# Kernel tuning notes

Hardware: AMD Instinct MI355X
Metric: run time of the kernel (lower is better)

## Reference

```python
import jax, jax.numpy as jnp
import numpy as np

IN_C, OUT_C, P, K, STRIDE = 256, 256, 4, 3, 1
PAD = (K - 1) // 2

def setup_inputs() -> dict:
    key = jax.random.key(0)
    k1, k2, k3 = jax.random.split(key, 3)
    x = jax.random.normal(k1, (32, IN_C, 64, 64), dtype=jnp.float32)
    # KxK weights for (i,j) pairs where the KxK branch is taken
    Wk = jax.random.normal(k2, (OUT_C, IN_C, K, K), dtype=jnp.float32) * 0.05
    # 1x1 weights (one scalar per (i,j) pair) for the pointwise branch
    W1 = jax.random.normal(k3, (OUT_C, IN_C), dtype=jnp.float32) * 0.05
    return {"x": x, "Wk": Wk, "W1": W1}

def _effective_weight(Wk, W1):
    # Branch selection: j < first_K uses (in_c + j - first_K) % P == 0,
    # else (j - first_K) % P == 0; both equal (j - first_K) mod P == 0
    # with nonnegative modulo, where first_K = i % in_c.
    i = jnp.arange(OUT_C)[:, None]
    j = jnp.arange(IN_C)[None, :]
    first_K = i % IN_C
    kxk_mask = ((j - first_K) % P == 0)  # [out, in] bool
    # 1x1 conv (pad 0, stride s) == center tap of a padded KxK conv (pad (K-1)/2, stride s)
    center = jnp.zeros((K, K), Wk.dtype).at[K // 2, K // 2].set(1.0)
    W_1x1_embedded = W1[:, :, None, None] * center  # [out, in, K, K]
    return jnp.where(kxk_mask[:, :, None, None], Wk, W_1x1_embedded)

def reference(x, Wk, W1):
    W_eff = _effective_weight(Wk, W1)
    out = jax.lax.conv_general_dilated(
        x, W_eff,
        window_strides=(STRIDE, STRIDE),
        padding=[(PAD, PAD), (PAD, PAD)],
        dimension_numbers=("NCHW", "OIHW", "NCHW"),
    )
    return out
```

## Files before the change

kernel.cpp:

```cpp
#include <hip/hip_runtime.h>
#include <hip/hip_bf16.h>


#define IN_C  256
#define OUT_C 256
#define HH    64
#define WW    64

typedef __attribute__((ext_vector_type(8))) short bf16x8;
typedef __attribute__((ext_vector_type(4))) float f32x4;

#define BARC() do {                                              \
        asm volatile("s_waitcnt lgkmcnt(0)" ::: "memory");       \
        __builtin_amdgcn_s_barrier();                            \
        __builtin_amdgcn_sched_barrier(0);                       \
    } while (0)

__device__ __forceinline__ unsigned short f2bf(float f) {
    union { float f; unsigned int u; } v; v.f = f;
    unsigned int r = (v.u + 0x7FFFu + ((v.u >> 16) & 1u)) >> 16;
    return (unsigned short)r;
}

__device__ __forceinline__ unsigned pkbf(float lo, float hi) {
    union { __hip_bfloat162 b; unsigned u; } c;
    c.b = __float22bfloat162_rn(make_float2(lo, hi));
    return c.u;
}

__global__ __launch_bounds__(256)
void hetconv_prep(const float* __restrict__ Wk, const float* __restrict__ W1,
                  unsigned short* __restrict__ ws16) {
    const int TOTAL = 65536 + 131072;
    for (int idx = blockIdx.x * 256 + threadIdx.x; idx < TOTAL; idx += gridDim.x * 256) {
        float f;
        if (idx < 65536) {
            int e = idx & 7, lane = (idx >> 3) & 63, m = (idx >> 9) & 15, ck = idx >> 13;
            int g = ck & 3, h2 = ck >> 2;
            int p = m * 16 + (lane & 15);
            int i = (lane >> 4) * 8 + e;
            int j = g + 4 * (32 * h2 + i);
            int oc = 4 * (p & 63) + (p >> 6);
            f = ((p >> 6) == g) ? Wk[(oc * IN_C + j) * 9 + 4] : W1[oc * IN_C + j];
        } else {
            int k2 = idx - 65536;
            int e = k2 & 7, lane = (k2 >> 3) & 63;
            int mrow = (k2 >> 9) & 1, bi = (k2 >> 10) & 1, tp = (k2 >> 11) & 3;
            int hf = (k2 >> 13) & 1, ck = k2 >> 14;
            int g = ck & 3, h2 = ck >> 2;
            int tf = hf * 4 + tp, tfull = tf < 4 ? tf : tf + 1;
            int lo = bi * 32 + mrow * 16 + (lane & 15);
            int i = (lane >> 4) * 8 + e;
            int oc = 4 * lo + g;
            int j = g + 4 * (32 * h2 + i);
            f = Wk[(oc * IN_C + j) * 9 + tfull];
        }
        ws16[idx] = f2bf(f);
    }
}

__device__ __forceinline__ void stage_x_loads(const float* __restrict__ x, int n, int y0,
                                              int ck, int t, float4 v[4][2]) {
    const int g = ck & 3, h2 = ck >> 2;
    #pragma unroll
    for (int it = 0; it < 4; ++it) {
        int tau = t + it * 256;
        int icp = tau & 15, q = (tau >> 4) & 15, r = tau >> 8;
        int i0 = icp * 2;
        int j0 = g + 4 * (32 * h2 + i0);
        int gy = y0 + r - 1;
        float4 z = {0.f, 0.f, 0.f, 0.f};
        v[it][0] = z; v[it][1] = z;
        if ((unsigned)gy < 64u) {
            const float* p0 = x + (((size_t)n * IN_C + j0) << 12) + (gy << 6) + (q << 2);
            v[it][0] = *(const float4*)p0;
            v[it][1] = *(const float4*)(p0 + 16384);
        }
    }
}

__device__ __forceinline__ void stage_x_writes(int t, float4 v[4][2], unsigned short* __restrict__ xb) {
    #pragma unroll
    for (int it = 0; it < 4; ++it) {
        int tau = t + it * 256;
        int icp = tau & 15, q = (tau >> 4) & 15, r = tau >> 8;
        int i0 = icp * 2;
        unsigned d0 = pkbf(v[it][0].x, v[it][1].x);
        unsigned d1 = pkbf(v[it][0].y, v[it][1].y);
        unsigned d2 = pkbf(v[it][0].z, v[it][1].z);
        unsigned d3 = pkbf(v[it][0].w, v[it][1].w);
        int rb = (r * 66 + q * 4 + 1) * 40 + i0;
        *(unsigned*)&xb[rb]        = d0;
        *(unsigned*)&xb[rb + 40]   = d1;
        *(unsigned*)&xb[rb + 80]   = d2;
        *(unsigned*)&xb[rb + 120]  = d3;
    }
}

__device__ __forceinline__ f32x4 mfma(bf16x8 a, bf16x8 b, f32x4 c) {
    return __builtin_amdgcn_mfma_f32_16x16x32_bf16(a, b, c, 0, 0, 0);
}

__device__ __forceinline__ void partA(const unsigned short* __restrict__ xb,
        const unsigned short* __restrict__ whs, f32x4 acc[8][4],
        int mrow, int ncol, int lrow, int kc, int l) {
    bf16x8 b[4];
    #pragma unroll
    for (int ni = 0; ni < 4; ++ni)
        b[ni] = *(const bf16x8*)&xb[((ncol + 1) * 66 + ni * 16 + lrow + 1) * 40 + kc * 8];
    #pragma unroll
    for (int mi = 0; mi < 8; ++mi) {
        bf16x8 a = *(const bf16x8*)&whs[(mrow + 2 * mi) * 512 + l * 8];
        #pragma unroll
        for (int ni = 0; ni < 4; ++ni)
            acc[mi][ni] = mfma(a, b[ni], acc[mi][ni]);
    }
}

template <int G, int HALF>
__device__ __forceinline__ void taps(const unsigned short* __restrict__ xb,
        const unsigned short* __restrict__ wks, f32x4 acc[8][4],
        int mrow, int ncol, int lrow, int kc, int l) {
    #pragma unroll
    for (int tp = 0; tp < 4; ++tp) {
        const int tfull = HALF ? tp + 5 : tp;
        const int dy = tfull / 3 - 1, dx = tfull % 3 - 1;
        bf16x8 a0 = *(const bf16x8*)&wks[((tp * 2 + 0) * 2 + mrow) * 512 + l * 8];
        bf16x8 a1 = *(const bf16x8*)&wks[((tp * 2 + 1) * 2 + mrow) * 512 + l * 8];
        #pragma unroll
        for (int ni = 0; ni < 4; ++ni) {
            bf16x8 bb = *(const bf16x8*)&xb[((ncol + 1 + dy) * 66 + ni * 16 + lrow + 1 + dx) * 40 + kc * 8];
            acc[2 * G + 0][ni] = mfma(a0, bb, acc[2 * G + 0][ni]);
            acc[2 * G + 1][ni] = mfma(a1, bb, acc[2 * G + 1][ni]);
        }
    }
}

__global__ __launch_bounds__(256, 2)
void hetconv_mfma(const float* __restrict__ x,
                  const unsigned short* __restrict__ wgt,
                  float* __restrict__ out) {
    __shared__ unsigned short xs [4 * 66 * 40];
    __shared__ unsigned short whs[8192];
    __shared__ unsigned short wks[8192];
    const int t    = threadIdx.x;
    const int l    = t & 63;
    const int w    = t >> 6;
    const int mrow = w & 1;
    const int ncol = w >> 1;
    const int lrow = l & 15;
    const int kc   = l >> 4;

    const int bid = blockIdx.x;
    const int n   = (bid & 7) * 4 + (bid >> 8);
    const int y0  = ((bid >> 3) & 31) * 2;

    const unsigned short* WHg = wgt;
    const unsigned short* WKg = wgt + 65536;

    f32x4 acc[8][4];
    #pragma unroll
    for (int mi = 0; mi < 8; ++mi)
        #pragma unroll
        for (int ni = 0; ni < 4; ++ni) acc[mi][ni] = (f32x4){0.f, 0.f, 0.f, 0.f};

    float4 xv[4][2];
    bf16x8 wv[8];

    stage_x_loads(x, n, y0, 0, t, xv);
    #pragma unroll
    for (int it = 0; it < 4; ++it) {
        wv[it]     = *(const bf16x8*)&WHg[(t + it * 256) * 8];
        wv[4 + it] = *(const bf16x8*)&WKg[(t + it * 256) * 8];
    }
    if (t < 128) {
        int r = t >> 5, side = (t >> 4) & 1, u = t & 15;
        *(unsigned*)&xs[(r * 66 + side * 65) * 40 + u * 2] = 0u;
    }
    stage_x_writes(t, xv, xs);
    #pragma unroll
    for (int it = 0; it < 4; ++it) {
        *(bf16x8*)&whs[(t + it * 256) * 8] = wv[it];
        *(bf16x8*)&wks[(t + it * 256) * 8] = wv[4 + it];
    }
    __syncthreads();

#define CHUNK(CK, LAST)                                                          \
    {                                                                            \
        bf16x8 wvb[4];                                                           \
        _Pragma("unroll")                                                        \
        for (int it = 0; it < 4; ++it)     \
            wvb[it] = *(const bf16x8*)&WKg[(CK) * 16384 + 8192 + (t + it * 256) * 8]; \
        partA(xs, whs, acc, mrow, ncol, lrow, kc, l);                            \
        taps<(CK) & 3, 0>(xs, wks, acc, mrow, ncol, lrow, kc, l);                \
        BARC();                                           \
        _Pragma("unroll")                                                        \
        for (int it = 0; it < 4; ++it)                                           \
            *(bf16x8*)&wks[(t + it * 256) * 8] = wvb[it];                        \
        if (!(LAST)) {                               \
            stage_x_loads(x, n, y0, (CK) + 1, t, xv);                            \
            _Pragma("unroll")                                                    \
            for (int it = 0; it < 4; ++it) {                                     \
                wv[it]     = *(const bf16x8*)&WHg[((CK) + 1) * 8192 + (t + it * 256) * 8]; \
                wv[4 + it] = *(const bf16x8*)&WKg[((CK) + 1) * 16384 + (t + it * 256) * 8]; \
            }                                                                    \
        }                                                                        \
        BARC();                                             \
        taps<(CK) & 3, 1>(xs, wks, acc, mrow, ncol, lrow, kc, l);                \
        if (!(LAST)) {                                                           \
            BARC();                                    \
            stage_x_writes(t, xv, xs);                                           \
            _Pragma("unroll")                                                    \
            for (int it = 0; it < 4; ++it) {                                     \
                *(bf16x8*)&whs[(t + it * 256) * 8] = wv[it];                     \
                *(bf16x8*)&wks[(t + it * 256) * 8] = wv[4 + it];                 \
            }                                                                    \
            __syncthreads();                                        \
        }                                                                        \
    }

    CHUNK(0, 0) CHUNK(1, 0) CHUNK(2, 0) CHUNK(3, 0)
    CHUNK(4, 0) CHUNK(5, 0) CHUNK(6, 0) CHUNK(7, 1)
#undef CHUNK

    #pragma unroll
    for (int mi = 0; mi < 8; ++mi) {
        int m = mrow + 2 * mi;
        #pragma unroll
        for (int ni = 0; ni < 4; ++ni) {
            #pragma unroll
            for (int reg = 0; reg < 4; ++reg) {
                int p  = m * 16 + kc * 4 + reg;
                int oc = 4 * (p & 63) + (p >> 6);
                out[(((size_t)n * OUT_C + oc) * HH + (y0 + ncol)) * WW + ni * 16 + lrow] = acc[mi][ni][reg];
            }
        }
    }
}

#define TH 16
#define TW 16
#define ICC 16
__global__ __launch_bounds__(256)
void hetconv_fp32(const float* __restrict__ x,
                  const float* __restrict__ Wk,
                  const float* __restrict__ W1,
                  float* __restrict__ out) {
    const int t    = threadIdx.x;
    const int g    = blockIdx.y;
    const int n    = blockIdx.z;
    const int tile = blockIdx.x;
    const int ty0  = (tile >> 2) * TH;
    const int tx0  = (tile & 3) * TW;
    const int ol = t & 7;
    const int pl = t >> 3;
    const int r  = pl >> 1;
    const int ch = (pl & 1) * 8;
    __shared__ __align__(16) float xsf[ICC * 18 * 20];
    __shared__ __align__(16) float w1s[ICC * 64];
    __shared__ __align__(16) float wksf[4 * 9 * 64];
    float acc[8][8];
    #pragma unroll
    for (int k = 0; k < 8; ++k)
        #pragma unroll
        for (int p = 0; p < 8; ++p) acc[k][p] = 0.f;
    for (int ic0 = 0; ic0 < IN_C; ic0 += ICC) {
        for (int idx = t; idx < ICC * 18 * 18; idx += 256) {
            int ic = idx / 324, rem = idx - ic * 324, rr = rem / 18, cc = rem - rr * 18;
            int gy = ty0 + rr - 1, gx = tx0 + cc - 1;
            float v = 0.f;
            if (gy >= 0 && gy < HH && gx >= 0 && gx < WW)
                v = x[(((size_t)n * IN_C + ic0 + ic) * HH + gy) * WW + gx];
            xsf[ic * 360 + rr * 20 + cc] = v;
        }
        for (int idx = t; idx < ICC * 64; idx += 256) {
            int ic = idx >> 6, o = idx & 63;
            w1s[idx] = W1[(g + 4 * o) * IN_C + ic0 + ic];
        }
        for (int idx = t; idx < 4 * 9 * 64; idx += 256) {
            int a = idx / 576, rem = idx - a * 576, tap = rem >> 6, o = rem & 63;
            wksf[idx] = Wk[((g + 4 * o) * IN_C + ic0 + g + 4 * a) * 9 + tap];
        }
        __syncthreads();
        for (int ic = 0; ic < ICC; ++ic) {
            if ((ic & 3) != g) {
                const float* rowp = &xsf[ic * 360 + (r + 1) * 20 + ch];
                float4 A = *(const float4*)rowp;
                float4 B = *(const float4*)(rowp + 4);
                float  c8 = rowp[8];
                float xv2[8] = {A.y, A.z, A.w, B.x, B.y, B.z, B.w, c8};
                const float* wp = &w1s[ic * 64 + ol * 8];
                float4 wA = *(const float4*)wp;
                float4 wB = *(const float4*)(wp + 4);
                float wv2[8] = {wA.x, wA.y, wA.z, wA.w, wB.x, wB.y, wB.z, wB.w};
                #pragma unroll
                for (int k = 0; k < 8; ++k)
                    #pragma unroll
                    for (int p = 0; p < 8; ++p) acc[k][p] += wv2[k] * xv2[p];
            } else {
                const int a = ic >> 2;
                #pragma unroll
                for (int dy = -1; dy <= 1; ++dy) {
                    const float* rowp = &xsf[ic * 360 + (r + 1 + dy) * 20 + ch];
                    float4 A = *(const float4*)rowp;
                    float4 B = *(const float4*)(rowp + 4);
                    float2 C = *(const float2*)(rowp + 8);
                    float seg[10] = {A.x, A.y, A.z, A.w, B.x, B.y, B.z, B.w, C.x, C.y};
                    #pragma unroll
                    for (int dxi = 0; dxi < 3; ++dxi) {
                        const float* wp = &wksf[(a * 9 + (dy + 1) * 3 + dxi) * 64 + ol * 8];
                        float4 wA = *(const float4*)wp;
                        float4 wB = *(const float4*)(wp + 4);
                        float wv2[8] = {wA.x, wA.y, wA.z, wA.w, wB.x, wB.y, wB.z, wB.w};
                        #pragma unroll
                        for (int k = 0; k < 8; ++k)
                            #pragma unroll
                            for (int p = 0; p < 8; ++p) acc[k][p] += wv2[k] * seg[p + dxi];
                    }
                }
            }
        }
        __syncthreads();
    }
    #pragma unroll
    for (int k = 0; k < 8; ++k) {
        int oc = g + 4 * (ol * 8 + k);
        size_t base = (((size_t)n * OUT_C + oc) * HH + (ty0 + r)) * WW + tx0 + ch;
        float4 v0 = {acc[k][0], acc[k][1], acc[k][2], acc[k][3]};
        float4 v1 = {acc[k][4], acc[k][5], acc[k][6], acc[k][7]};
        *(float4*)(&out[base])     = v0;
        *(float4*)(&out[base + 4]) = v1;
    }
}

extern "C" void kernel_launch(void* const* d_in, const int* in_sizes, int n_in,
                              void* d_out, int out_size, void* d_ws, size_t ws_size,
                              hipStream_t stream) {
    const float* x  = (const float*)d_in[0];
    const float* Wk = (const float*)d_in[1];
    const float* W1 = (const float*)d_in[2];
    float* outp = (float*)d_out;

    if (ws_size >= (size_t)(65536 + 131072) * sizeof(unsigned short)) {
        hetconv_prep<<<256, 256, 0, stream>>>(Wk, W1, (unsigned short*)d_ws);
        hetconv_mfma<<<1024, 256, 0, stream>>>(x, (const unsigned short*)d_ws, outp);
    } else {
        hetconv_fp32<<<dim3(16, 4, 32), 256, 0, stream>>>(x, Wk, W1, outp);
    }
}
```

Before: 118.1 us.

## Shrink LDS x-tile pitch, split B-fragment loads, and restructure chunk staging

```diff
diff --git a/kernel.cpp b/kernel.cpp
--- a/kernel.cpp
+++ b/kernel.cpp
@@ -8,13 +8,8 @@
 #define WW    64
 
 typedef __attribute__((ext_vector_type(8))) short bf16x8;
+typedef __attribute__((ext_vector_type(4))) short bf16x4;
 typedef __attribute__((ext_vector_type(4))) float f32x4;
-
-#define BARC() do {                                              \
-        asm volatile("s_waitcnt lgkmcnt(0)" ::: "memory");       \
-        __builtin_amdgcn_s_barrier();                            \
-        __builtin_amdgcn_sched_barrier(0);                       \
-    } while (0)
 
 __device__ __forceinline__ unsigned short f2bf(float f) {
     union { float f; unsigned int u; } v; v.f = f;
@@ -59,6 +54,9 @@
     }
 }
 
+#define XSPAD 36
+#define XSSZ  (4 * 66 * XSPAD)
+
 __device__ __forceinline__ void stage_x_loads(const float* __restrict__ x, int n, int y0,
                                               int ck, int t, float4 v[4][2]) {
     const int g = ck & 3, h2 = ck >> 2;
@@ -89,12 +87,18 @@
         unsigned d1 = pkbf(v[it][0].y, v[it][1].y);
         unsigned d2 = pkbf(v[it][0].z, v[it][1].z);
         unsigned d3 = pkbf(v[it][0].w, v[it][1].w);
-        int rb = (r * 66 + q * 4 + 1) * 40 + i0;
-        *(unsigned*)&xb[rb]        = d0;
-        *(unsigned*)&xb[rb + 40]   = d1;
-        *(unsigned*)&xb[rb + 80]   = d2;
-        *(unsigned*)&xb[rb + 120]  = d3;
-    }
+        int rb = (r * 66 + q * 4 + 1) * XSPAD + i0;
+        *(unsigned*)&xb[rb]             = d0;
+        *(unsigned*)&xb[rb + XSPAD]     = d1;
+        *(unsigned*)&xb[rb + 2 * XSPAD] = d2;
+        *(unsigned*)&xb[rb + 3 * XSPAD] = d3;
+    }
+}
+
+__device__ __forceinline__ bf16x8 lds_bfrag(const unsigned short* __restrict__ xb, int off) {
+    bf16x4 lo = *(const bf16x4*)&xb[off];
+    bf16x4 hi = *(const bf16x4*)&xb[off + 4];
+    return __builtin_shufflevector(lo, hi, 0, 1, 2, 3, 4, 5, 6, 7);
 }
 
 __device__ __forceinline__ f32x4 mfma(bf16x8 a, bf16x8 b, f32x4 c) {
@@ -107,7 +111,7 @@
     bf16x8 b[4];
     #pragma unroll
     for (int ni = 0; ni < 4; ++ni)
-        b[ni] = *(const bf16x8*)&xb[((ncol + 1) * 66 + ni * 16 + lrow + 1) * 40 + kc * 8];
+        b[ni] = lds_bfrag(xb, ((ncol + 1) * 66 + ni * 16 + lrow + 1) * XSPAD + kc * 8);
     #pragma unroll
     for (int mi = 0; mi < 8; ++mi) {
         bf16x8 a = *(const bf16x8*)&whs[(mrow + 2 * mi) * 512 + l * 8];
@@ -129,7 +133,7 @@
         bf16x8 a1 = *(const bf16x8*)&wks[((tp * 2 + 1) * 2 + mrow) * 512 + l * 8];
         #pragma unroll
         for (int ni = 0; ni < 4; ++ni) {
-            bf16x8 bb = *(const bf16x8*)&xb[((ncol + 1 + dy) * 66 + ni * 16 + lrow + 1 + dx) * 40 + kc * 8];
+            bf16x8 bb = lds_bfrag(xb, ((ncol + 1 + dy) * 66 + ni * 16 + lrow + 1 + dx) * XSPAD + kc * 8);
             acc[2 * G + 0][ni] = mfma(a0, bb, acc[2 * G + 0][ni]);
             acc[2 * G + 1][ni] = mfma(a1, bb, acc[2 * G + 1][ni]);
         }
@@ -140,7 +144,7 @@
 void hetconv_mfma(const float* __restrict__ x,
                   const unsigned short* __restrict__ wgt,
                   float* __restrict__ out) {
-    __shared__ unsigned short xs [4 * 66 * 40];
+    __shared__ unsigned short xs [XSSZ];
     __shared__ unsigned short whs[8192];
     __shared__ unsigned short wks[8192];
     const int t    = threadIdx.x;
@@ -164,59 +168,44 @@
         #pragma unroll
         for (int ni = 0; ni < 4; ++ni) acc[mi][ni] = (f32x4){0.f, 0.f, 0.f, 0.f};
 
-    float4 xv[4][2];
-    bf16x8 wv[8];
-
-    stage_x_loads(x, n, y0, 0, t, xv);
-    #pragma unroll
-    for (int it = 0; it < 4; ++it) {
-        wv[it]     = *(const bf16x8*)&WHg[(t + it * 256) * 8];
-        wv[4 + it] = *(const bf16x8*)&WKg[(t + it * 256) * 8];
-    }
     if (t < 128) {
         int r = t >> 5, side = (t >> 4) & 1, u = t & 15;
-        *(unsigned*)&xs[(r * 66 + side * 65) * 40 + u * 2] = 0u;
-    }
-    stage_x_writes(t, xv, xs);
-    #pragma unroll
-    for (int it = 0; it < 4; ++it) {
-        *(bf16x8*)&whs[(t + it * 256) * 8] = wv[it];
-        *(bf16x8*)&wks[(t + it * 256) * 8] = wv[4 + it];
-    }
-    __syncthreads();
+        *(unsigned*)&xs[(r * 66 + side * 65) * XSPAD + u * 2] = 0u;
+    }
+    float4 xv[4][2];
+    stage_x_loads(x, n, y0, 0, t, xv);
 
 #define CHUNK(CK, LAST)                                                          \
     {                                                                            \
+        __syncthreads();                      \
+        bf16x8 wv[8];                                                            \
+        _Pragma("unroll")                                                        \
+        for (int it = 0; it < 4; ++it) {              \
+            int e = (t + it * 256) * 8;                                          \
+            wv[it]     = *(const bf16x8*)&WHg[(CK) * 8192 + e];                  \
+            wv[4 + it] = *(const bf16x8*)&WKg[(CK) * 16384 + e];                 \
+        }                                                                        \
+        stage_x_writes(t, xv, xs);            \
+        _Pragma("unroll")                                                        \
+        for (int it = 0; it < 4; ++it) {                                         \
+            int e = (t + it * 256) * 8;                                          \
+            *(bf16x8*)&whs[e] = wv[it];                                          \
+            *(bf16x8*)&wks[e] = wv[4 + it];                                      \
+        }                                                                        \
+        __syncthreads();                              \
         bf16x8 wvb[4];                                                           \
         _Pragma("unroll")                                                        \
-        for (int it = 0; it < 4; ++it)     \
+        for (int it = 0; it < 4; ++it)          \
             wvb[it] = *(const bf16x8*)&WKg[(CK) * 16384 + 8192 + (t + it * 256) * 8]; \
         partA(xs, whs, acc, mrow, ncol, lrow, kc, l);                            \
         taps<(CK) & 3, 0>(xs, wks, acc, mrow, ncol, lrow, kc, l);                \
-        BARC();                                           \
+        __syncthreads();                                 \
         _Pragma("unroll")                                                        \
         for (int it = 0; it < 4; ++it)                                           \
             *(bf16x8*)&wks[(t + it * 256) * 8] = wvb[it];                        \
-        if (!(LAST)) {                               \
-            stage_x_loads(x, n, y0, (CK) + 1, t, xv);                            \
-            _Pragma("unroll")                                                    \
-            for (int it = 0; it < 4; ++it) {                                     \
-                wv[it]     = *(const bf16x8*)&WHg[((CK) + 1) * 8192 + (t + it * 256) * 8]; \
-                wv[4 + it] = *(const bf16x8*)&WKg[((CK) + 1) * 16384 + (t + it * 256) * 8]; \
-            }                                                                    \
-        }                                                                        \
-        BARC();                                             \
+        if (!(LAST)) stage_x_loads(x, n, y0, (CK) + 1, t, xv);                   \
+        __syncthreads();                                      \
         taps<(CK) & 3, 1>(xs, wks, acc, mrow, ncol, lrow, kc, l);                \
-        if (!(LAST)) {                                                           \
-            BARC();                                    \
-            stage_x_writes(t, xv, xs);                                           \
-            _Pragma("unroll")                                                    \
-            for (int it = 0; it < 4; ++it) {                                     \
-                *(bf16x8*)&whs[(t + it * 256) * 8] = wv[it];                     \
-                *(bf16x8*)&wks[(t + it * 256) * 8] = wv[4 + it];                 \
-            }                                                                    \
-            __syncthreads();                                        \
-        }                                                                        \
     }
 
     CHUNK(0, 0) CHUNK(1, 0) CHUNK(2, 0) CHUNK(3, 0)
```

New measurement: 107.5 us. 9.0% less time.
